# Performance work log

Hardware: AMD Instinct MI355X
Metric: run time of the kernel (lower is better)

## Reference

```python
import jax, jax.numpy as jnp
import numpy as np

N_NODES = 50000
N_EDGES = 800000
IN_C = 64
HID = 128
OUT_C = 2
N_GRAPHS = 64


def setup_inputs() -> dict:
    key = jax.random.key(0)
    ks = jax.random.split(key, 12)
    x = jax.random.normal(ks[0], (N_NODES, IN_C), dtype=jnp.float32)
    edge_index = jax.random.randint(ks[1], (2, N_EDGES), 0, N_NODES, dtype=jnp.int64)
    batch = jnp.sort(jax.random.randint(ks[2], (N_NODES,), 0, N_GRAPHS, dtype=jnp.int64))
    def glorot(k, shape):
        lim = float(np.sqrt(6.0 / (shape[0] + shape[1])))
        return jax.random.uniform(k, shape, dtype=jnp.float32, minval=-lim, maxval=lim)
    return {
        "x": x,
        "edge_index": edge_index,
        "batch": batch,
        "W1": glorot(ks[3], (IN_C, HID)),  "b1": jnp.zeros((HID,), jnp.float32),
        "W2": glorot(ks[4], (HID, HID)),   "b2": jnp.zeros((HID,), jnp.float32),
        "Wm1": glorot(ks[5], (HID, HID)),  "bm1": jnp.zeros((HID,), jnp.float32),
        "Wm2": glorot(ks[6], (HID, OUT_C)), "bm2": jnp.zeros((OUT_C,), jnp.float32),
    }


def reference(x, edge_index, batch, W1, b1, W2, b2, Wm1, bm1, Wm2, bm2):
    N = x.shape[0]
    # GCN normalization with self-loops (PyG GCNConv defaults)
    loops = jnp.arange(N, dtype=edge_index.dtype)
    src = jnp.concatenate([edge_index[0], loops])  # message sources
    dst = jnp.concatenate([edge_index[1], loops])  # aggregation targets
    deg = jax.ops.segment_sum(jnp.ones(dst.shape, x.dtype), dst, num_segments=N)
    dinv = jnp.where(deg > 0, jax.lax.rsqrt(deg), 0.0)
    norm = dinv[src] * dinv[dst]  # [E+N]

    def gcn_conv(h, W, b):
        h = h @ W                         # transform first (PyG order)
        msg = h[src] * norm[:, None]      # gather + normalize
        return jax.ops.segment_sum(msg, dst, num_segments=N) + b  # scatter-add

    h = jax.nn.relu(gcn_conv(x, W1, b1))
    # dropout is identity in eval mode
    h = gcn_conv(h, W2, b2)

    # global mean pool over graphs
    sums = jax.ops.segment_sum(h, batch, num_segments=N_GRAPHS)
    cnt = jax.ops.segment_sum(jnp.ones((N,), h.dtype), batch, num_segments=N_GRAPHS)
    g = sums / jnp.maximum(cnt, 1.0)[:, None]  # [G, HID]

    g = jax.nn.relu(g @ Wm1 + bm1)
    return g @ Wm2 + bm2  # [G, OUT_C]
```

## Files before the change

### kernel.cpp

```cpp
#include <hip/hip_runtime.h>
#include <stdint.h>

#define N_NODES 50000
#define N_EDGES 800000
#define IN_C 64
#define HID 128
#define OUT_C 2
#define N_GRAPHS 64
#define NBUCK 196
#define BCAP 6144
#define ECH 4096

typedef long long i64;
typedef __attribute__((ext_vector_type(8))) short bf8;
typedef __attribute__((ext_vector_type(4))) float f32x4;

__device__ __forceinline__ float bf2f(ushort h) {
    return __uint_as_float(((uint)h) << 16);
}
__device__ __forceinline__ ushort f2bf(float f) {
    uint x = __float_as_uint(f);
    uint r = x + 0x7fffu + ((x >> 16) & 1u);
    return (ushort)(r >> 16);
}
__device__ __forceinline__ float loadf(const void* p, size_t i, int bf) {
    return bf ? bf2f(((const ushort*)p)[i]) : ((const float*)p)[i];
}
__device__ __forceinline__ int clampi(int v, int lo, int hi) {
    return min(max(v, lo), hi);
}

__device__ __forceinline__ int edge_src(const void* ei, int e, int wide) {
    return wide ? (int)((const i64*)ei)[e] : ((const int*)ei)[e];
}
__device__ __forceinline__ int edge_dst(const void* ei, int e, int wide) {
    return wide ? (int)((const i64*)ei)[N_EDGES + e] : ((const int*)ei)[N_EDGES + e];
}
__device__ __forceinline__ i64 batch_at(const void* b, int i, int wide) {
    return wide ? ((const i64*)b)[i] : (i64)((const int*)b)[i];
}

__device__ __forceinline__ void bset(float* a, uint4 u) {
    a[0] = bf2f((ushort)(u.x & 0xffffu)); a[1] = bf2f((ushort)(u.x >> 16));
    a[2] = bf2f((ushort)(u.y & 0xffffu)); a[3] = bf2f((ushort)(u.y >> 16));
    a[4] = bf2f((ushort)(u.z & 0xffffu)); a[5] = bf2f((ushort)(u.z >> 16));
    a[6] = bf2f((ushort)(u.w & 0xffffu)); a[7] = bf2f((ushort)(u.w >> 16));
}
__device__ __forceinline__ void bacc(float* a, uint4 u) {
    a[0] += bf2f((ushort)(u.x & 0xffffu)); a[1] += bf2f((ushort)(u.x >> 16));
    a[2] += bf2f((ushort)(u.y & 0xffffu)); a[3] += bf2f((ushort)(u.y >> 16));
    a[4] += bf2f((ushort)(u.z & 0xffffu)); a[5] += bf2f((ushort)(u.z >> 16));
    a[6] += bf2f((ushort)(u.w & 0xffffu)); a[7] += bf2f((ushort)(u.w >> 16));
}
__device__ __forceinline__ uint pk2(float lo, float hi) {
    return ((uint)f2bf(hi) << 16) | (uint)f2bf(lo);
}
__device__ __forceinline__ bf8 packbf8(const float* a, float dv) {
    union { bf8 v; uint u[4]; } r;
    r.u[0] = pk2(a[0] * dv, a[1] * dv);
    r.u[1] = pk2(a[2] * dv, a[3] * dv);
    r.u[2] = pk2(a[4] * dv, a[5] * dv);
    r.u[3] = pk2(a[6] * dv, a[7] * dv);
    return r.v;
}

__global__ __launch_bounds__(256) void k_init(const uint* __restrict__ braw,
                                              const uint* __restrict__ xraw,
                                              int* __restrict__ bcnt,
                                              float* __restrict__ gbuf,
                                              int* __restrict__ iflag,
                                              int* __restrict__ fflag) {
    int i = blockIdx.x * blockDim.x + threadIdx.x;
    if (i < N_GRAPHS * HID) gbuf[i] = 0.f;
    if (i < NBUCK) bcnt[i] = 0;
    if (blockIdx.x == 0) {
        __shared__ uint si[128];
        __shared__ int sf[256];
        int t = threadIdx.x;
        if (t < 128) si[t] = (t < 100) ? braw[25001 + 2 * t] : 0u;
        uint e = (xraw[t] >> 7) & 0xFFu;
        sf[t] = (e >= 100u && e <= 140u) ? 1 : 0;
        __syncthreads();
        for (int off = 128; off > 0; off >>= 1) {
            if (t < off) {
                sf[t] += sf[t + off];
                if (off <= 64 && t < 64) si[t] |= si[t + off];
            }
            __syncthreads();
        }
        if (t == 0) {
            *iflag = (si[0] == 0u) ? 1 : 0;
            *fflag = (sf[0] >= 192) ? 1 : 0;
        }
    }
}

__global__ __launch_bounds__(1024) void k_binA(const void* __restrict__ ei,
                                               const int* __restrict__ iflag,
                                               const int* __restrict__ fflag,
                                               const void* __restrict__ W1,
                                               const void* __restrict__ W2,
                                               ushort* __restrict__ Wt1,
                                               ushort* __restrict__ Wt2,
                                               int* __restrict__ bcnt,
                                               uint2* __restrict__ bmem) {
    int t = threadIdx.x;
    if (t < 256 && blockIdx.x < (IN_C * HID + HID * HID) / 256) {
        int ff = *fflag;
        int idx = blockIdx.x * 256 + t;
        if (idx < IN_C * HID) {
            int k = idx >> 7, n = idx & 127;
            Wt1[n * IN_C + k] = f2bf(loadf(W1, idx, ff));
        } else {
            int j = idx - IN_C * HID;
            int k = j >> 7, n = j & 127;
            Wt2[n * HID + k] = f2bf(loadf(W2, j, ff));
        }
    }
    int wide = *iflag;
    __shared__ int cnt[NBUCK];
    __shared__ int obase[NBUCK];
    __shared__ int run[NBUCK];
    __shared__ int gbase[NBUCK];
    __shared__ int sc[256];
    __shared__ uint2 stage[ECH];
    int e0 = blockIdx.x * ECH;
    int m = min(ECH, N_EDGES - e0);
    for (int i = t; i < NBUCK; i += 1024) cnt[i] = 0;
    __syncthreads();
    for (int i = t; i < m; i += 1024) {
        int d = edge_dst(ei, e0 + i, wide);
        atomicAdd(&cnt[d >> 8], 1);
    }
    __syncthreads();
    int cv = (t < NBUCK) ? cnt[t] : 0;
    if (t < 256) sc[t] = cv;
    __syncthreads();
    for (int off = 1; off < 256; off <<= 1) {
        int v = (t >= off && t < 256) ? sc[t - off] : 0;
        __syncthreads();
        if (t < 256) sc[t] += v;
        __syncthreads();
    }
    if (t < NBUCK) {
        int ex = sc[t] - cv;
        obase[t] = ex;
        run[t] = ex;
        gbase[t] = (cv > 0) ? atomicAdd(&bcnt[t], cv) : 0;
    }
    __syncthreads();
    for (int i = t; i < m; i += 1024) {
        int s = edge_src(ei, e0 + i, wide);
        int d = edge_dst(ei, e0 + i, wide);
        int slot = atomicAdd(&run[d >> 8], 1);
        uint2 pr; pr.x = (uint)s; pr.y = (uint)d;
        stage[slot] = pr;
    }
    __syncthreads();
    for (int i = t; i < m; i += 1024) {
        uint2 pr = stage[i];
        int b = (int)(pr.y >> 8);
        int pos = gbase[b] + (i - obase[b]);
        if (pos < BCAP) bmem[(size_t)b * BCAP + pos] = pr;
    }
}

__global__ __launch_bounds__(1024) void k_binB(const uint2* __restrict__ bmem,
                                               const int* __restrict__ bcnt,
                                               const void* __restrict__ x,
                                               const int* __restrict__ fflag,
                                               int* __restrict__ offs,
                                               int* __restrict__ csr,
                                               float* __restrict__ dinv,
                                               ushort* __restrict__ Y1) {
    int b = blockIdx.x;
    int t = threadIdx.x;
    int node0 = b << 8;
    __shared__ int sc[256];
    __shared__ int degl[256];
    __shared__ int run[256];
    __shared__ float sdinv[256];
    __shared__ int sbase, scnt;
    __shared__ int stage[BCAP];
    int v = (t < NBUCK) ? bcnt[t] : 0;
    if (t < 256) sc[t] = v;
    __syncthreads();
    for (int off = 1; off < 256; off <<= 1) {
        int u = (t >= off && t < 256) ? sc[t - off] : 0;
        __syncthreads();
        if (t < 256) sc[t] += u;
        __syncthreads();
    }
    if (t == b) {
        int c = clampi(v, 0, BCAP);
        scnt = c;
        sbase = clampi(sc[t] - v, 0, N_EDGES - c);
    }
    if (t < 256) degl[t] = 0;
    __syncthreads();
    int cnt = scnt;
    int base = sbase;
    for (int i = t; i < cnt; i += 1024) {
        uint2 pr = bmem[(size_t)b * BCAP + i];
        atomicAdd(&degl[pr.y & 255], 1);
    }
    __syncthreads();
    int dv = (t < 256) ? degl[t] : 0;
    if (t < 256) sc[t] = dv;
    __syncthreads();
    for (int off = 1; off < 256; off <<= 1) {
        int u = (t >= off && t < 256) ? sc[t - off] : 0;
        __syncthreads();
        if (t < 256) sc[t] += u;
        __syncthreads();
    }
    if (t < 256) {
        int ex = sc[t] - dv;
        run[t] = ex;
        float di = rsqrtf((float)(dv + 1));
        sdinv[t] = di;
        int n = node0 + t;
        if (n < N_NODES) { offs[n] = base + ex; dinv[n] = di; }
    }
    if (b == 0 && t == 0) offs[N_NODES] = N_EDGES;
    __syncthreads();
    for (int i = t; i < cnt; i += 1024) {
        uint2 pr = bmem[(size_t)b * BCAP + i];
        int slot = atomicAdd(&run[pr.y & 255], 1);
        stage[clampi(slot, 0, BCAP - 1)] = (int)pr.x;
    }
    __syncthreads();
    for (int i = t; i < cnt; i += 1024) csr[base + i] = stage[i];
    int ff = *fflag;
    for (int idx = t; idx < 256 * (IN_C / 4); idx += 1024) {
        int nl = idx >> 4, c4 = (idx & 15) * 4;
        int nn = node0 + nl;
        if (nn < N_NODES) {
            float x0, x1, x2, x3;
            if (ff) {
                ushort4 u = *(const ushort4*)((const ushort*)x + (size_t)nn * IN_C + c4);
                x0 = bf2f(u.x); x1 = bf2f(u.y); x2 = bf2f(u.z); x3 = bf2f(u.w);
            } else {
                float4 vv = *(const float4*)((const float*)x + (size_t)nn * IN_C + c4);
                x0 = vv.x; x1 = vv.y; x2 = vv.z; x3 = vv.w;
            }
            float di = sdinv[nl];
            ushort4 o;
            o.x = f2bf(x0 * di); o.y = f2bf(x1 * di);
            o.z = f2bf(x2 * di); o.w = f2bf(x3 * di);
            *(ushort4*)(Y1 + (size_t)nn * IN_C + c4) = o;
        }
    }
}

__global__ __launch_bounds__(256) void k_l1(const ushort* __restrict__ Y1,
                                            const float* __restrict__ dinv,
                                            const int* __restrict__ offs,
                                            const int* __restrict__ csr,
                                            const ushort* __restrict__ Wt,
                                            const int* __restrict__ fflag,
                                            const void* __restrict__ bias,
                                            ushort* __restrict__ out) {
    int ff = *fflag;
    int wave = threadIdx.x >> 6;
    int lane = threadIdx.x & 63;
    int m16 = lane & 15;
    int q = lane >> 4;
    int rowbase = blockIdx.x * 64 + wave * 16;
    int n = min(rowbase + m16, N_NODES - 1);

    const uint4* y4 = (const uint4*)Y1;
    size_t rb = (size_t)n * 8 + q;
    float a0[8], a1[8];
    bset(a0, y4[rb]);
    bset(a1, y4[rb + 4]);
    int s = offs[n];
    int e = min(offs[n + 1], s + 4096);
    int i = s;
    for (; i + 4 <= e; i += 4) {
        uint4 u[4][2];
#pragma unroll
        for (int k = 0; k < 4; k++) {
            size_t r = (size_t)csr[i + k] * 8 + q;
            u[k][0] = y4[r];
            u[k][1] = y4[r + 4];
        }
#pragma unroll
        for (int k = 0; k < 4; k++) { bacc(a0, u[k][0]); bacc(a1, u[k][1]); }
    }
    for (; i < e; i++) {
        size_t r = (size_t)csr[i] * 8 + q;
        bacc(a0, y4[r]);
        bacc(a1, y4[r + 4]);
    }
    float dvn = dinv[n];
    bf8 af0 = packbf8(a0, dvn);
    bf8 af1 = packbf8(a1, dvn);

    f32x4 acc[8];
#pragma unroll
    for (int t = 0; t < 8; t++) acc[t] = (f32x4){0.f, 0.f, 0.f, 0.f};
#pragma unroll
    for (int t = 0; t < 8; t++) {
        bf8 b0 = *(const bf8*)(Wt + (size_t)(t * 16 + m16) * IN_C + q * 8);
        acc[t] = __builtin_amdgcn_mfma_f32_16x16x32_bf16(af0, b0, acc[t], 0, 0, 0);
        bf8 b1 = *(const bf8*)(Wt + (size_t)(t * 16 + m16) * IN_C + 32 + q * 8);
        acc[t] = __builtin_amdgcn_mfma_f32_16x16x32_bf16(af1, b1, acc[t], 0, 0, 0);
    }
    float dv[4];
    int rowok[4];
#pragma unroll
    for (int r = 0; r < 4; r++) {
        int row = rowbase + q * 4 + r;
        rowok[r] = (row < N_NODES);
        dv[r] = rowok[r] ? dinv[row] : 1.f;
    }
#pragma unroll
    for (int t = 0; t < 8; t++) {
        int col = t * 16 + m16;
        float bv = loadf(bias, col, ff);
#pragma unroll
        for (int r = 0; r < 4; r++) {
            int row = rowbase + q * 4 + r;
            if (rowok[r]) {
                float v = fmaxf(acc[t][r] + bv, 0.f) * dv[r];
                out[(size_t)row * HID + col] = f2bf(v);
            }
        }
    }
}

__global__ __launch_bounds__(256) void k_l2(const ushort* __restrict__ hs,
                                            const float* __restrict__ dinv,
                                            const int* __restrict__ offs,
                                            const int* __restrict__ csr,
                                            const ushort* __restrict__ Wt,
                                            const void* __restrict__ batch,
                                            const int* __restrict__ iflag,
                                            float* __restrict__ gsum) {
    int wide = *iflag;
    int tid = threadIdx.x;
    int wave = tid >> 6;
    int lane = tid & 63;
    int m16 = lane & 15;
    int q = lane >> 4;
    int rowbase = blockIdx.x * 64 + wave * 16;
    int n = min(rowbase + m16, N_NODES - 1);

    __shared__ float sacc[64][HID];
    __shared__ int sbg[64];
    if (tid < 64) {
        int nn = blockIdx.x * 64 + tid;
        int g = (nn < N_NODES) ? (int)batch_at(batch, nn, wide) : -1;
        sbg[tid] = (g < 0 || g >= N_GRAPHS) ? -1 : g;
    }

    const uint4* h4 = (const uint4*)hs;
    size_t rb = (size_t)n * 16 + q;
    float a[4][8];
    bset(a[0], h4[rb]);
    bset(a[1], h4[rb + 4]);
    bset(a[2], h4[rb + 8]);
    bset(a[3], h4[rb + 12]);
    int s = offs[n];
    int e = min(offs[n + 1], s + 4096);
    int i = s;
    for (; i + 2 <= e; i += 2) {
        uint4 u[2][4];
#pragma unroll
        for (int kk = 0; kk < 2; kk++) {
            size_t r = (size_t)csr[i + kk] * 16 + q;
            u[kk][0] = h4[r];
            u[kk][1] = h4[r + 4];
            u[kk][2] = h4[r + 8];
            u[kk][3] = h4[r + 12];
        }
#pragma unroll
        for (int kk = 0; kk < 2; kk++) {
#pragma unroll
            for (int k = 0; k < 4; k++) bacc(a[k], u[kk][k]);
        }
    }
    for (; i < e; i++) {
        size_t r = (size_t)csr[i] * 16 + q;
        bacc(a[0], h4[r]);
        bacc(a[1], h4[r + 4]);
        bacc(a[2], h4[r + 8]);
        bacc(a[3], h4[r + 12]);
    }
    float dvn = dinv[n];
    bf8 af0 = packbf8(a[0], dvn);
    bf8 af1 = packbf8(a[1], dvn);
    bf8 af2 = packbf8(a[2], dvn);
    bf8 af3 = packbf8(a[3], dvn);

    f32x4 acc[8];
#pragma unroll
    for (int t = 0; t < 8; t++) acc[t] = (f32x4){0.f, 0.f, 0.f, 0.f};
#pragma unroll
    for (int t = 0; t < 8; t++) {
        const ushort* wr = Wt + (size_t)(t * 16 + m16) * HID + q * 8;
        acc[t] = __builtin_amdgcn_mfma_f32_16x16x32_bf16(af0, *(const bf8*)(wr), acc[t], 0, 0, 0);
        acc[t] = __builtin_amdgcn_mfma_f32_16x16x32_bf16(af1, *(const bf8*)(wr + 32), acc[t], 0, 0, 0);
        acc[t] = __builtin_amdgcn_mfma_f32_16x16x32_bf16(af2, *(const bf8*)(wr + 64), acc[t], 0, 0, 0);
        acc[t] = __builtin_amdgcn_mfma_f32_16x16x32_bf16(af3, *(const bf8*)(wr + 96), acc[t], 0, 0, 0);
    }
#pragma unroll
    for (int t = 0; t < 8; t++) {
        int col = t * 16 + m16;
#pragma unroll
        for (int r = 0; r < 4; r++) {
            int rl = wave * 16 + q * 4 + r;
            int row = rowbase + q * 4 + r;
            sacc[rl][col] = (row < N_NODES) ? acc[t][r] : 0.f;
        }
    }
    __syncthreads();
    int col = tid & 127;
    int half = tid >> 7;
    int gcur = -1;
    float av = 0.f;
    for (int r = half * 32; r < half * 32 + 32; r++) {
        int g = sbg[r];
        if (g != gcur) {
            if (gcur >= 0) atomicAdd(&gsum[gcur * HID + col], av);
            av = 0.f;
            gcur = g;
        }
        av += sacc[r][col];
    }
    if (gcur >= 0) atomicAdd(&gsum[gcur * HID + col], av);
}

__global__ void k_mlp(const float* __restrict__ gsum, const void* __restrict__ batch,
                      const int* __restrict__ iflag, const void* __restrict__ b2,
                      const void* __restrict__ Wm1, const void* __restrict__ bm1,
                      const void* __restrict__ Wm2, const void* __restrict__ bm2,
                      const int* __restrict__ fflag, float* __restrict__ out) {
    int ff = *fflag;
    int wide = *iflag;
    int gr = blockIdx.x;
    int c = threadIdx.x;
    int lo = 0, hi = N_NODES;
    while (lo < hi) { int m = (lo + hi) >> 1; if (batch_at(batch, m, wide) < (i64)gr) lo = m + 1; else hi = m; }
    int s = lo;
    lo = s; hi = N_NODES;
    while (lo < hi) { int m = (lo + hi) >> 1; if (batch_at(batch, m, wide) < (i64)(gr + 1)) lo = m + 1; else hi = m; }
    float cnt = (float)(lo - s);

    __shared__ float sg[HID];
    __shared__ float r0[HID], r1[HID];
    sg[c] = gsum[gr * HID + c] / fmaxf(cnt, 1.0f) + loadf(b2, c, ff);
    __syncthreads();
    float acc = loadf(bm1, c, ff);
#pragma unroll 8
    for (int k = 0; k < HID; k++) acc += sg[k] * loadf(Wm1, k * HID + c, ff);
    float hid = fmaxf(acc, 0.f);
    r0[c] = hid * loadf(Wm2, c * OUT_C + 0, ff);
    r1[c] = hid * loadf(Wm2, c * OUT_C + 1, ff);
    __syncthreads();
    for (int off = 64; off > 0; off >>= 1) {
        if (c < off) { r0[c] += r0[c + off]; r1[c] += r1[c + off]; }
        __syncthreads();
    }
    if (c == 0) {
        out[gr * OUT_C + 0] = r0[0] + loadf(bm2, 0, ff);
        out[gr * OUT_C + 1] = r1[0] + loadf(bm2, 1, ff);
    }
}


extern "C" void kernel_launch(void* const* d_in, const int* in_sizes, int n_in,
                              void* d_out, int out_size, void* d_ws, size_t ws_size,
                              hipStream_t stream) {
    const void* x     = d_in[0];
    const void* ei    = d_in[1];
    const void* batch = d_in[2];
    const void* W1  = d_in[3];
    const void* b1  = d_in[4];
    const void* W2  = d_in[5];
    const void* b2  = d_in[6];
    const void* Wm1 = d_in[7];
    const void* bm1 = d_in[8];
    const void* Wm2 = d_in[9];
    const void* bm2 = d_in[10];

    char* p = (char*)d_ws;
    auto alloc = [&](size_t bytes) {
        char* r = p;
        p += (bytes + 255) & ~(size_t)255;
        return r;
    };
    int*    iflag  = (int*)alloc(4);
    int*    fflag  = (int*)alloc(4);
    int*    bcnt   = (int*)alloc(NBUCK * 4);
    uint2*  bmem   = (uint2*)alloc((size_t)NBUCK * BCAP * 8);
    float*  dinv   = (float*)alloc(N_NODES * 4);
    int*    offs   = (int*)alloc((N_NODES + 1) * 4);
    int*    csr    = (int*)alloc(N_EDGES * 4);
    ushort* Wt1    = (ushort*)alloc(IN_C * HID * 2);
    ushort* Wt2    = (ushort*)alloc(HID * HID * 2);
    ushort* Y1     = (ushort*)alloc((size_t)N_NODES * IN_C * 2);
    ushort* h1s    = (ushort*)alloc((size_t)N_NODES * HID * 2);
    float*  gbuf   = (float*)alloc(N_GRAPHS * HID * 4);

    k_init<<<(N_GRAPHS * HID + 255) / 256, 256, 0, stream>>>(
        (const uint*)batch, (const uint*)x, bcnt, gbuf, iflag, fflag);
    k_binA<<<(N_EDGES + ECH - 1) / ECH, 1024, 0, stream>>>(
        ei, iflag, fflag, W1, W2, Wt1, Wt2, bcnt, bmem);
    k_binB<<<NBUCK, 1024, 0, stream>>>(bmem, bcnt, x, fflag, offs, csr, dinv, Y1);

    k_l1<<<(N_NODES + 63) / 64, 256, 0, stream>>>(Y1, dinv, offs, csr, Wt1, fflag, b1, h1s);
    k_l2<<<(N_NODES + 63) / 64, 256, 0, stream>>>(h1s, dinv, offs, csr, Wt2, batch, iflag, gbuf);

    k_mlp<<<N_GRAPHS, HID, 0, stream>>>(gbuf, batch, iflag, b2, Wm1, bm1, Wm2, bm2, fflag, (float*)d_out);
}
```

Measured before the change: 209.7 us.

## Fold layer-2 aggregation and mean pool into a per-node graph-weight matrix

Because layer 2 is linear and is followed directly by mean pooling, the pooled result can be written as a weighted sum of h1 rows with per-source graph weights, followed by one W2 multiply per graph. The change builds a dense N_NODES×N_GRAPHS weight matrix by scattering atomics during CSR construction and replaces the gather-based layer-2 kernel with a small dense contraction. W2 is then applied inside the MLP kernel. This drops 800K row gathers of h1 and the MFMA pass, but adds zeroing and reading a 12.8 MB matrix plus 800K global float atomics.

```diff
diff --git a/kernel.cpp b/kernel.cpp
--- a/kernel.cpp
+++ b/kernel.cpp
@@ -10,6 +10,7 @@
 #define NBUCK 196
 #define BCAP 6144
 #define ECH 4096
+#define PCH 128
 
 typedef long long i64;
 typedef __attribute__((ext_vector_type(8))) short bf8;
@@ -68,11 +69,15 @@
                                               const uint* __restrict__ xraw,
                                               int* __restrict__ bcnt,
                                               float* __restrict__ gbuf,
+                                              float* __restrict__ WT,
                                               int* __restrict__ iflag,
                                               int* __restrict__ fflag) {
     int i = blockIdx.x * blockDim.x + threadIdx.x;
     if (i < N_GRAPHS * HID) gbuf[i] = 0.f;
     if (i < NBUCK) bcnt[i] = 0;
+    float4 z = make_float4(0.f, 0.f, 0.f, 0.f);
+    for (int j = i; j < N_NODES * 16; j += gridDim.x * blockDim.x)
+        ((float4*)WT)[j] = z;
     if (blockIdx.x == 0) {
         __shared__ uint si[128];
         __shared__ int sf[256];
@@ -99,23 +104,15 @@
                                                const int* __restrict__ iflag,
                                                const int* __restrict__ fflag,
                                                const void* __restrict__ W1,
-                                               const void* __restrict__ W2,
                                                ushort* __restrict__ Wt1,
-                                               ushort* __restrict__ Wt2,
                                                int* __restrict__ bcnt,
                                                uint2* __restrict__ bmem) {
     int t = threadIdx.x;
-    if (t < 256 && blockIdx.x < (IN_C * HID + HID * HID) / 256) {
+    if (t < 256 && blockIdx.x < (IN_C * HID) / 256) {
         int ff = *fflag;
         int idx = blockIdx.x * 256 + t;
-        if (idx < IN_C * HID) {
-            int k = idx >> 7, n = idx & 127;
-            Wt1[n * IN_C + k] = f2bf(loadf(W1, idx, ff));
-        } else {
-            int j = idx - IN_C * HID;
-            int k = j >> 7, n = j & 127;
-            Wt2[n * HID + k] = f2bf(loadf(W2, j, ff));
-        }
+        int k = idx >> 7, n = idx & 127;
+        Wt1[n * IN_C + k] = f2bf(loadf(W1, idx, ff));
     }
     int wide = *iflag;
     __shared__ int cnt[NBUCK];
@@ -168,18 +165,23 @@
 __global__ __launch_bounds__(1024) void k_binB(const uint2* __restrict__ bmem,
                                                const int* __restrict__ bcnt,
                                                const void* __restrict__ x,
+                                               const void* __restrict__ batch,
+                                               const int* __restrict__ iflag,
                                                const int* __restrict__ fflag,
                                                int* __restrict__ offs,
                                                int* __restrict__ csr,
                                                float* __restrict__ dinv,
+                                               float* __restrict__ WT,
                                                ushort* __restrict__ Y1) {
     int b = blockIdx.x;
     int t = threadIdx.x;
     int node0 = b << 8;
+    int wide = *iflag;
     __shared__ int sc[256];
     __shared__ int degl[256];
     __shared__ int run[256];
     __shared__ float sdinv[256];
+    __shared__ int sgb[256];
     __shared__ int sbase, scnt;
     __shared__ int stage[BCAP];
     int v = (t < NBUCK) ? bcnt[t] : 0;
@@ -220,14 +222,24 @@
         float di = rsqrtf((float)(dv + 1));
         sdinv[t] = di;
         int n = node0 + t;
-        if (n < N_NODES) { offs[n] = base + ex; dinv[n] = di; }
+        if (n < N_NODES) {
+            offs[n] = base + ex;
+            dinv[n] = di;
+            int g = clampi((int)batch_at(batch, n, wide), 0, N_GRAPHS - 1);
+            sgb[t] = g;
+            atomicAdd(&WT[(size_t)n * N_GRAPHS + g], di);
+        } else {
+            sgb[t] = 0;
+        }
     }
     if (b == 0 && t == 0) offs[N_NODES] = N_EDGES;
     __syncthreads();
     for (int i = t; i < cnt; i += 1024) {
         uint2 pr = bmem[(size_t)b * BCAP + i];
-        int slot = atomicAdd(&run[pr.y & 255], 1);
+        int dl = pr.y & 255;
+        int slot = atomicAdd(&run[dl], 1);
         stage[clampi(slot, 0, BCAP - 1)] = (int)pr.x;
+        atomicAdd(&WT[(size_t)pr.x * N_GRAPHS + sgb[dl]], sdinv[dl]);
     }
     __syncthreads();
     for (int i = t; i < cnt; i += 1024) csr[base + i] = stage[i];
@@ -330,110 +342,57 @@
     }
 }
 
-__global__ __launch_bounds__(256) void k_l2(const ushort* __restrict__ hs,
-                                            const float* __restrict__ dinv,
-                                            const int* __restrict__ offs,
-                                            const int* __restrict__ csr,
-                                            const ushort* __restrict__ Wt,
-                                            const void* __restrict__ batch,
-                                            const int* __restrict__ iflag,
-                                            float* __restrict__ gsum) {
-    int wide = *iflag;
-    int tid = threadIdx.x;
-    int wave = tid >> 6;
-    int lane = tid & 63;
-    int m16 = lane & 15;
-    int q = lane >> 4;
-    int rowbase = blockIdx.x * 64 + wave * 16;
-    int n = min(rowbase + m16, N_NODES - 1);
-
-    __shared__ float sacc[64][HID];
-    __shared__ int sbg[64];
-    if (tid < 64) {
-        int nn = blockIdx.x * 64 + tid;
-        int g = (nn < N_NODES) ? (int)batch_at(batch, nn, wide) : -1;
-        sbg[tid] = (g < 0 || g >= N_GRAPHS) ? -1 : g;
-    }
-
-    const uint4* h4 = (const uint4*)hs;
-    size_t rb = (size_t)n * 16 + q;
-    float a[4][8];
-    bset(a[0], h4[rb]);
-    bset(a[1], h4[rb + 4]);
-    bset(a[2], h4[rb + 8]);
-    bset(a[3], h4[rb + 12]);
-    int s = offs[n];
-    int e = min(offs[n + 1], s + 4096);
-    int i = s;
-    for (; i + 2 <= e; i += 2) {
-        uint4 u[2][4];
-#pragma unroll
-        for (int kk = 0; kk < 2; kk++) {
-            size_t r = (size_t)csr[i + kk] * 16 + q;
-            u[kk][0] = h4[r];
-            u[kk][1] = h4[r + 4];
-            u[kk][2] = h4[r + 8];
-            u[kk][3] = h4[r + 12];
-        }
-#pragma unroll
-        for (int kk = 0; kk < 2; kk++) {
-#pragma unroll
-            for (int k = 0; k < 4; k++) bacc(a[k], u[kk][k]);
-        }
-    }
-    for (; i < e; i++) {
-        size_t r = (size_t)csr[i] * 16 + q;
-        bacc(a[0], h4[r]);
-        bacc(a[1], h4[r + 4]);
-        bacc(a[2], h4[r + 8]);
-        bacc(a[3], h4[r + 12]);
-    }
-    float dvn = dinv[n];
-    bf8 af0 = packbf8(a[0], dvn);
-    bf8 af1 = packbf8(a[1], dvn);
-    bf8 af2 = packbf8(a[2], dvn);
-    bf8 af3 = packbf8(a[3], dvn);
-
-    f32x4 acc[8];
-#pragma unroll
-    for (int t = 0; t < 8; t++) acc[t] = (f32x4){0.f, 0.f, 0.f, 0.f};
-#pragma unroll
-    for (int t = 0; t < 8; t++) {
-        const ushort* wr = Wt + (size_t)(t * 16 + m16) * HID + q * 8;
-        acc[t] = __builtin_amdgcn_mfma_f32_16x16x32_bf16(af0, *(const bf8*)(wr), acc[t], 0, 0, 0);
-        acc[t] = __builtin_amdgcn_mfma_f32_16x16x32_bf16(af1, *(const bf8*)(wr + 32), acc[t], 0, 0, 0);
-        acc[t] = __builtin_amdgcn_mfma_f32_16x16x32_bf16(af2, *(const bf8*)(wr + 64), acc[t], 0, 0, 0);
-        acc[t] = __builtin_amdgcn_mfma_f32_16x16x32_bf16(af3, *(const bf8*)(wr + 96), acc[t], 0, 0, 0);
-    }
-#pragma unroll
-    for (int t = 0; t < 8; t++) {
-        int col = t * 16 + m16;
-#pragma unroll
-        for (int r = 0; r < 4; r++) {
-            int rl = wave * 16 + q * 4 + r;
-            int row = rowbase + q * 4 + r;
-            sacc[rl][col] = (row < N_NODES) ? acc[t][r] : 0.f;
-        }
-    }
-    __syncthreads();
-    int col = tid & 127;
-    int half = tid >> 7;
-    int gcur = -1;
-    float av = 0.f;
-    for (int r = half * 32; r < half * 32 + 32; r++) {
-        int g = sbg[r];
-        if (g != gcur) {
-            if (gcur >= 0) atomicAdd(&gsum[gcur * HID + col], av);
-            av = 0.f;
-            gcur = g;
-        }
-        av += sacc[r][col];
-    }
-    if (gcur >= 0) atomicAdd(&gsum[gcur * HID + col], av);
+__global__ __launch_bounds__(256) void k_pool2(const float* __restrict__ WT,
+                                               const ushort* __restrict__ hs,
+                                               float* __restrict__ gsum) {
+    __shared__ float4 sW[PCH * 16];
+    __shared__ uint4  sH[PCH * 16];
+    int t = threadIdx.x;
+    int s0 = blockIdx.x * PCH;
+    const float4* w4 = (const float4*)WT;
+    const uint4*  h4 = (const uint4*)hs;
+    for (int idx = t; idx < PCH * 16; idx += 256) {
+        int row = idx >> 4;
+        int nn = s0 + row;
+        if (nn < N_NODES) {
+            sW[idx] = w4[(size_t)nn * 16 + (idx & 15)];
+            sH[idx] = h4[(size_t)nn * 16 + (idx & 15)];
+        } else {
+            sW[idx] = make_float4(0.f, 0.f, 0.f, 0.f);
+            sH[idx] = make_uint4(0u, 0u, 0u, 0u);
+        }
+    }
+    __syncthreads();
+    int tc = t & 15;
+    int tg = t >> 4;
+    float acc[4][8];
+#pragma unroll
+    for (int gi = 0; gi < 4; gi++)
+#pragma unroll
+        for (int ci = 0; ci < 8; ci++) acc[gi][ci] = 0.f;
+    for (int s = 0; s < PCH; s++) {
+        float4 w = sW[s * 16 + tg];
+        uint4 hq = sH[s * 16 + tc];
+        float h[8];
+        bset(h, hq);
+        float wv[4] = {w.x, w.y, w.z, w.w};
+#pragma unroll
+        for (int gi = 0; gi < 4; gi++) {
+#pragma unroll
+            for (int ci = 0; ci < 8; ci++) acc[gi][ci] += wv[gi] * h[ci];
+        }
+    }
+    int gb = 4 * tg, cb = 8 * tc;
+#pragma unroll
+    for (int gi = 0; gi < 4; gi++)
+#pragma unroll
+        for (int ci = 0; ci < 8; ci++)
+            atomicAdd(&gsum[(gb + gi) * HID + cb + ci], acc[gi][ci]);
 }
 
 __global__ void k_mlp(const float* __restrict__ gsum, const void* __restrict__ batch,
-                      const int* __restrict__ iflag, const void* __restrict__ b2,
+                      const int* __restrict__ iflag, const void* __restrict__ W2,
+                      const void* __restrict__ b2,
                       const void* __restrict__ Wm1, const void* __restrict__ bm1,
                       const void* __restrict__ Wm2, const void* __restrict__ bm2,
                       const int* __restrict__ fflag, float* __restrict__ out) {
@@ -448,9 +407,15 @@
     while (lo < hi) { int m = (lo + hi) >> 1; if (batch_at(batch, m, wide) < (i64)(gr + 1)) lo = m + 1; else hi = m; }
     float cnt = (float)(lo - s);
 
+    __shared__ float st[HID];
     __shared__ float sg[HID];
     __shared__ float r0[HID], r1[HID];
-    sg[c] = gsum[gr * HID + c] / fmaxf(cnt, 1.0f) + loadf(b2, c, ff);
+    st[c] = gsum[gr * HID + c];
+    __syncthreads();
+    float v = 0.f;
+#pragma unroll 8
+    for (int k = 0; k < HID; k++) v += st[k] * loadf(W2, (size_t)k * HID + c, ff);
+    sg[c] = v / fmaxf(cnt, 1.0f) + loadf(b2, c, ff);
     __syncthreads();
     float acc = loadf(bm1, c, ff);
 #pragma unroll 8
@@ -499,19 +464,20 @@
     int*    offs   = (int*)alloc((N_NODES + 1) * 4);
     int*    csr    = (int*)alloc(N_EDGES * 4);
     ushort* Wt1    = (ushort*)alloc(IN_C * HID * 2);
-    ushort* Wt2    = (ushort*)alloc(HID * HID * 2);
+    float*  WT     = (float*)alloc((size_t)N_NODES * N_GRAPHS * 4);
     ushort* Y1     = (ushort*)alloc((size_t)N_NODES * IN_C * 2);
     ushort* h1s    = (ushort*)alloc((size_t)N_NODES * HID * 2);
     float*  gbuf   = (float*)alloc(N_GRAPHS * HID * 4);
 
-    k_init<<<(N_GRAPHS * HID + 255) / 256, 256, 0, stream>>>(
-        (const uint*)batch, (const uint*)x, bcnt, gbuf, iflag, fflag);
+    k_init<<<1024, 256, 0, stream>>>(
+        (const uint*)batch, (const uint*)x, bcnt, gbuf, WT, iflag, fflag);
     k_binA<<<(N_EDGES + ECH - 1) / ECH, 1024, 0, stream>>>(
-        ei, iflag, fflag, W1, W2, Wt1, Wt2, bcnt, bmem);
-    k_binB<<<NBUCK, 1024, 0, stream>>>(bmem, bcnt, x, fflag, offs, csr, dinv, Y1);
+        ei, iflag, fflag, W1, Wt1, bcnt, bmem);
+    k_binB<<<NBUCK, 1024, 0, stream>>>(bmem, bcnt, x, batch, iflag, fflag,
+                                       offs, csr, dinv, WT, Y1);
 
     k_l1<<<(N_NODES + 63) / 64, 256, 0, stream>>>(Y1, dinv, offs, csr, Wt1, fflag, b1, h1s);
-    k_l2<<<(N_NODES + 63) / 64, 256, 0, stream>>>(h1s, dinv, offs, csr, Wt2, batch, iflag, gbuf);
-
-    k_mlp<<<N_GRAPHS, HID, 0, stream>>>(gbuf, batch, iflag, b2, Wm1, bm1, Wm2, bm2, fflag, (float*)d_out);
-}
+    k_pool2<<<(N_NODES + PCH - 1) / PCH, 256, 0, stream>>>(WT, h1s, gbuf);
+
+    k_mlp<<<N_GRAPHS, HID, 0, stream>>>(gbuf, batch, iflag, W2, b2, Wm1, bm1, Wm2, bm2, fflag, (float*)d_out);
+}
```

Result: slower. 321.2 us (+53.2%).
